# Kernel tuning notes

Hardware: AMD Instinct MI355X
Metric: run time of the kernel (lower is better)

The kernel has to match this reference:

```python
import jax, jax.numpy as jnp
import numpy as np

K = 8
TEMP = 0.05
EPS = 1e-8


def setup_inputs() -> dict:
    key = jax.random.key(0)
    k1, k2, k3, k4, k5, k6 = jax.random.split(key, 6)
    N, D, H = 8192, 1024, 64
    h0 = jax.random.normal(k1, (N, D), dtype=jnp.float32)
    coords = jax.random.uniform(k2, (N, 2), dtype=jnp.float32)
    # tiny MLP params: Linear(2,H) -> ReLU -> Linear(H,1) -> Sigmoid
    W1 = jax.random.normal(k3, (2, H), dtype=jnp.float32) * (1.0 / np.sqrt(2))
    b1 = jnp.zeros((H,), dtype=jnp.float32)
    W2 = jax.random.normal(k4, (H, 1), dtype=jnp.float32) * (1.0 / np.sqrt(H))
    b2 = jnp.zeros((1,), dtype=jnp.float32)
    return {"h0": h0, "coords": coords, "W1": W1, "b1": b1, "W2": W2, "b2": b2}


def reference(h0, coords, W1, b1, W2, b2):
    # pairwise euclidean distances [N, N]
    sq = jnp.sum(coords * coords, axis=-1)                      # [N]
    d2 = sq[:, None] + sq[None, :] - 2.0 * (coords @ coords.T)  # [N, N]
    dist = jnp.sqrt(jnp.maximum(d2, 0.0))

    # k+1 nearest (smallest dist), drop self (index 0)
    _, idx = jax.lax.top_k(-dist, K + 1)                        # [N, K+1]
    knn_idx = idx[:, 1:]                                        # [N, K]

    # gather neighbor features [N, K, D]
    neighbor_feats = h0[knn_idx]

    # cosine similarity between h_i and each neighbor (torch eps semantics)
    num = jnp.einsum('nd,nkd->nk', h0, neighbor_feats)          # [N, K]
    ni = jnp.maximum(jnp.linalg.norm(h0, axis=-1), EPS)         # [N]
    nj = jnp.maximum(jnp.linalg.norm(neighbor_feats, axis=-1), EPS)  # [N, K]
    sim = num / (ni[:, None] * nj)

    # spatial weights from gathered distances
    d_knn = jnp.take_along_axis(dist, knn_idx, axis=1)          # [N, K]
    spatial_w = jnp.exp(-d_knn / TEMP)

    density_input = jnp.stack(
        [sim.mean(axis=1), spatial_w.mean(axis=1)], axis=1)     # [N, 2]

    hmid = jax.nn.relu(density_input @ W1 + b1)
    density = jax.nn.sigmoid(hmid @ W2 + b2)                    # [N, 1]
    return density
```

## Files before the change

### kernel.cpp

```cpp
#include <hip/hip_runtime.h>
#include <math.h>

#define NROWS 8192
#define DIM   1024
#define GRID  64
#define CELLW 0.015625f
#define LPR   16

__device__ __forceinline__ int cell_of(float v) {
    int c = (int)(v * 64.0f);
    return c < 0 ? 0 : (c > 63 ? 63 : c);
}

__device__ __forceinline__ float np_d2(float xi, float yi, float sqi,
                                       float xj, float yj) {
    float sqj = __fadd_rn(__fmul_rn(xj, xj), __fmul_rn(yj, yj));
    float G   = fmaf(yi, yj, __fmul_rn(xi, xj));
    return __fsub_rn(__fadd_rn(sqi, sqj), __fmul_rn(2.0f, G));
}

__global__ __launch_bounds__(1024) void build_grid_kernel(
    const float* __restrict__ coords,
    int* __restrict__ cellStart,
    float4* __restrict__ sxyz) {

    __shared__ int lcnt[4096];
    __shared__ int wsum[16];
    const int t = threadIdx.x;

    for (int i = t; i < 4096; i += 1024) lcnt[i] = 0;
    __syncthreads();

    float2 pc[8]; int pcell[8];
#pragma unroll
    for (int k = 0; k < 8; ++k) {
        int i = t + 1024 * k;
        float2 c = ((const float2*)coords)[i];
        pc[k] = c;
        pcell[k] = cell_of(c.y) * GRID + cell_of(c.x);
        atomicAdd(&lcnt[pcell[k]], 1);
    }
    __syncthreads();

    int c0 = lcnt[t*4+0], c1 = lcnt[t*4+1], c2 = lcnt[t*4+2], c3 = lcnt[t*4+3];
    int s1 = c0, s2 = c0 + c1, s3 = s2 + c2, s4 = s3 + c3;
    int lane = t & 63, wid = t >> 6;
    int inc = s4;
#pragma unroll
    for (int off = 1; off < 64; off <<= 1) {
        int o = __shfl_up(inc, off, 64);
        if (lane >= off) inc += o;
    }
    if (lane == 63) wsum[wid] = inc;
    __syncthreads();
    int wbase = 0;
    for (int w = 0; w < wid; ++w) wbase += wsum[w];
    int excl = wbase + inc - s4;

    cellStart[t*4+0] = excl;
    cellStart[t*4+1] = excl + s1;
    cellStart[t*4+2] = excl + s2;
    cellStart[t*4+3] = excl + s3;
    if (t == 1023) cellStart[4096] = excl + s4;
    lcnt[t*4+0] = excl;
    lcnt[t*4+1] = excl + s1;
    lcnt[t*4+2] = excl + s2;
    lcnt[t*4+3] = excl + s3;
    __syncthreads();

#pragma unroll
    for (int k = 0; k < 8; ++k) {
        int pos = atomicAdd(&lcnt[pcell[k]], 1);
        float x = pc[k].x, y = pc[k].y;
        float sq = __fadd_rn(__fmul_rn(x, x), __fmul_rn(y, y));
        sxyz[pos] = make_float4(x, y, sq, __int_as_float(t + 1024 * k));
    }
}

__global__ __launch_bounds__(256) void knn_kernel(
    const int* __restrict__ cellStart,
    const float4* __restrict__ sxyz,
    unsigned long long* __restrict__ chosen_ws) {

    const int sub = threadIdx.x & (LPR - 1);
    const int g   = (blockIdx.x * 256 + threadIdx.x) / LPR;

    const float4 me = sxyz[g];
    const float xi = me.x, yi = me.y, sqi = me.z;
    const int row = __float_as_int(me.w);
    const int cx = cell_of(xi), cy = cell_of(yi);

    unsigned long long best[10], merged[10];
    int C = 2;
    while (true) {
#pragma unroll
        for (int s = 0; s < 10; ++s) best[s] = ~0ULL;
        int x0 = max(0, cx - C), x1 = min(GRID - 1, cx + C);
        int y0 = max(0, cy - C), y1 = min(GRID - 1, cy + C);
        for (int yy = y0; yy <= y1; ++yy) {
            int s = cellStart[yy * GRID + x0];
            int e = cellStart[yy * GRID + x1 + 1];
            for (int t = s + sub; t < e; t += LPR) {
                float4 c = sxyz[t];
                float d2  = __fsub_rn(__fadd_rn(sqi, c.z),
                                      __fmul_rn(2.0f, fmaf(yi, c.y, __fmul_rn(xi, c.x))));
                float dst = __fsqrt_rn(fmaxf(d2, 0.0f));
                unsigned long long key =
                    ((unsigned long long)__float_as_uint(dst) << 32)
                    | (unsigned int)__float_as_int(c.w);
                if (key < best[9]) {
                    best[9] = key;
#pragma unroll
                    for (int ss = 9; ss >= 1; --ss) {
                        unsigned long long a = best[ss - 1], b = best[ss];
                        unsigned long long lo = a < b ? a : b;
                        unsigned long long hi = a < b ? b : a;
                        best[ss - 1] = lo;
                        best[ss]     = hi;
                    }
                }
            }
        }
#pragma unroll
        for (int r = 0; r < 10; ++r) {
            unsigned long long mn = best[0];
#pragma unroll
            for (int off = 1; off < LPR; off <<= 1) {
                unsigned long long o = __shfl_xor(mn, off, 64);
                mn = (o < mn) ? o : mn;
            }
            if (best[0] == mn) {
#pragma unroll
                for (int ss = 0; ss < 9; ++ss) best[ss] = best[ss + 1];
                best[9] = ~0ULL;
            }
            merged[r] = mn;
        }
        bool done = false;
        if (merged[9] != ~0ULL) {
            float d9 = __uint_as_float((unsigned int)(merged[9] >> 32));
            if (d9 + 1.0e-3f <= (float)C * CELLW) done = true;
        }
        if (done || C >= GRID) break;
        C <<= 1; if (C > GRID) C = GRID;
    }

    if (sub == 0) {
        unsigned long long* o = chosen_ws + (size_t)row * 10;
#pragma unroll
        for (int r = 0; r < 10; ++r) o[r] = merged[r];
    }
}

__global__ __launch_bounds__(256) void gather_final_kernel(
    const float* __restrict__ h0,
    const float* __restrict__ coords,
    const unsigned long long* __restrict__ chosen_ws,
    const float4* __restrict__ sxyz,
    const float* __restrict__ W1, const float* __restrict__ b1,
    const float* __restrict__ W2, const float* __restrict__ b2,
    float* __restrict__ out) {

    const int wid  = threadIdx.x >> 6;
    const int lane = threadIdx.x & 63;
    const int bid  = blockIdx.x;
    const int grp  = (bid & 7) * (gridDim.x / 8) + (bid >> 3);
    const int g    = grp * 4 + wid;
    const int row  = __float_as_int(sxyz[g].w);

    const unsigned long long* ch = chosen_ws + (size_t)row * 10;
    unsigned long long chosen[10];
    int jidx[10];
#pragma unroll
    for (int r = 0; r < 10; ++r) {
        chosen[r] = ch[r];
        jidx[r]   = (int)(chosen[r] & 0xFFFFFFFFu);
    }

    const float4* hi = (const float4*)(h0 + (size_t)row * DIM);

    float p[11];
    float q[10];
#pragma unroll
    for (int s = 0; s < 11; ++s) p[s] = 0.f;
#pragma unroll
    for (int s = 0; s < 10; ++s) q[s] = 0.f;

    for (int t = 0; t < 4; ++t) {
        float4 av = hi[lane + 64 * t];
        p[10] += av.x * av.x + av.y * av.y + av.z * av.z + av.w * av.w;
#pragma unroll
        for (int s = 0; s < 10; ++s) {
            float4 b = ((const float4*)(h0 + (size_t)jidx[s] * DIM))[lane + 64 * t];
            p[s] += av.x * b.x + av.y * b.y + av.z * b.z + av.w * b.w;
            q[s] += b.x * b.x + b.y * b.y + b.z * b.z + b.w * b.w;
        }
    }

#pragma unroll
    for (int s = 0; s < 11; ++s) {
        float v = p[s];
#pragma unroll
        for (int off = 1; off < 64; off <<= 1) v += __shfl_xor(v, off, 64);
        p[s] = v;
    }
#pragma unroll
    for (int s = 0; s < 10; ++s) {
        float v = q[s];
#pragma unroll
        for (int off = 1; off < 64; off <<= 1) v += __shfl_xor(v, off, 64);
        q[s] = v;
    }

    const float2 ci = ((const float2*)coords)[row];
    const float xi = ci.x, yi = ci.y;
    const float sqi = __fadd_rn(__fmul_rn(xi, xi), __fmul_rn(yi, yi));

    auto clamped_d2 = [&](unsigned long long key) -> float {
        int j = (int)(key & 0xFFFFFFFFu);
        float2 cj = ((const float2*)coords)[j];
        return fmaxf(np_d2(xi, yi, sqi, cj.x, cj.y), 0.0f);
    };
    const float m0 = clamped_d2(chosen[0]);
    const float m1 = clamped_d2(chosen[1]);
    const float m2 = clamped_d2(chosen[2]);
    const float m8 = clamped_d2(chosen[8]);
    const float m9 = clamped_d2(chosen[9]);

    const float WIN = 2.0e-6f;
    const bool fpair = (m1 - m0) <= WIN;
    const bool ftri  = fpair && ((m2 - m0) <= WIN);
    const bool f89   = (m9 - m8) <= WIN;

    float wd[3];
    wd[0] = ftri ? (1.f / 3.f) : (fpair ? 0.5f : 1.0f);
    wd[1] = ftri ? (1.f / 3.f) : (fpair ? 0.5f : 0.0f);
    wd[2] = ftri ? (1.f / 3.f) : 0.0f;
    const float wc0 = f89 ? 0.5f : 1.0f;
    const float wc1 = f89 ? 0.5f : 0.0f;

    const float ni = fmaxf(sqrtf(p[10]), 1e-8f);

    float sim[10], sw[10];
#pragma unroll
    for (int r = 0; r < 10; ++r) {
        float dst = __uint_as_float((unsigned int)(chosen[r] >> 32));
        float nj  = fmaxf(sqrtf(q[r]), 1e-8f);
        sim[r] = p[r] / (ni * nj);
        sw[r]  = expf(__fdiv_rn(-dst, 0.05f));
    }

    float Ssim = 0.f, Ssw = 0.f;
#pragma unroll
    for (int r = 0; r < 9; ++r) { Ssim += sim[r]; Ssw += sw[r]; }

    const float w1a = W1[lane], w1b = W1[64 + lane];
    const float b1l = b1[lane], w2l = W2[lane], b2s = b2[0];

    float outacc = 0.f;
#pragma unroll
    for (int d = 0; d < 3; ++d) {
#pragma unroll
        for (int c = 0; c < 2; ++c) {
            float wgt = wd[d] * (c ? wc1 : wc0);
            float simsum = Ssim - sim[d] + (c ? (sim[9] - sim[8]) : 0.f);
            float swsum  = Ssw  - sw[d]  + (c ? (sw[9]  - sw[8])  : 0.f);
            float di0 = simsum * 0.125f;
            float di1 = swsum  * 0.125f;
            float hm = fmaxf(di0 * w1a + di1 * w1b + b1l, 0.f);
            float v  = hm * w2l;
#pragma unroll
            for (int off = 1; off < 64; off <<= 1) v += __shfl_xor(v, off, 64);
            float z = v + b2s;
            outacc += wgt * (1.f / (1.f + expf(-z)));
        }
    }

    if (lane == 0) out[row] = outacc;
}

extern "C" void kernel_launch(void* const* d_in, const int* in_sizes, int n_in,
                              void* d_out, int out_size, void* d_ws, size_t ws_size,
                              hipStream_t stream) {
    const float* h0     = (const float*)d_in[0];
    const float* coords = (const float*)d_in[1];
    const float* W1     = (const float*)d_in[2];
    const float* b1     = (const float*)d_in[3];
    const float* W2     = (const float*)d_in[4];
    const float* b2     = (const float*)d_in[5];
    float* out = (float*)d_out;

    char* ws = (char*)d_ws;
    unsigned long long* chosen_ws = (unsigned long long*)(ws);
    float4* sxyz      = (float4*)(ws + 1015808);
    int*    cellStart = (int*)(ws + 1146880);

    build_grid_kernel  <<<1, 1024, 0, stream>>>(coords, cellStart, sxyz);
    knn_kernel         <<<NROWS * LPR / 256, 256, 0, stream>>>(cellStart, sxyz, chosen_ws);
    gather_final_kernel<<<NROWS / 4, 256, 0, stream>>>(h0, coords, chosen_ws, sxyz,
                                                       W1, b1, W2, b2, out);
}
```

Baseline: 58.37 us.

## Precompute row norms inside knn kernel and drop neighbor norm reductions in gather

```diff
diff --git a/kernel.cpp b/kernel.cpp
--- a/kernel.cpp
+++ b/kernel.cpp
@@ -78,9 +78,31 @@
 }
 
 __global__ __launch_bounds__(256) void knn_kernel(
+    const float* __restrict__ h0,
     const int* __restrict__ cellStart,
     const float4* __restrict__ sxyz,
-    unsigned long long* __restrict__ chosen_ws) {
+    unsigned long long* __restrict__ chosen_ws,
+    float* __restrict__ norms) {
+
+    {
+        const int wv   = threadIdx.x >> 6;
+        const int lane = threadIdx.x & 63;
+        int rbase = blockIdx.x * 16 + wv * 4;
+#pragma unroll
+        for (int k = 0; k < 4; ++k) {
+            int row = rbase + k;
+            const float4* hp = (const float4*)(h0 + (size_t)row * DIM);
+            float acc = 0.f;
+#pragma unroll
+            for (int t = 0; t < 4; ++t) {
+                float4 v = hp[lane + 64 * t];
+                acc += v.x * v.x + v.y * v.y + v.z * v.z + v.w * v.w;
+            }
+#pragma unroll
+            for (int off = 1; off < 64; off <<= 1) acc += __shfl_xor(acc, off, 64);
+            if (lane == 0) norms[row] = sqrtf(acc);
+        }
+    }
 
     const int sub = threadIdx.x & (LPR - 1);
     const int g   = (blockIdx.x * 256 + threadIdx.x) / LPR;
@@ -157,6 +179,7 @@
     const float* __restrict__ coords,
     const unsigned long long* __restrict__ chosen_ws,
     const float4* __restrict__ sxyz,
+    const float* __restrict__ norms,
     const float* __restrict__ W1, const float* __restrict__ b1,
     const float* __restrict__ W2, const float* __restrict__ b2,
     float* __restrict__ out) {
@@ -170,46 +193,35 @@
 
     const unsigned long long* ch = chosen_ws + (size_t)row * 10;
     unsigned long long chosen[10];
-    int jidx[10];
+    const float4* hj[10];
 #pragma unroll
     for (int r = 0; r < 10; ++r) {
         chosen[r] = ch[r];
-        jidx[r]   = (int)(chosen[r] & 0xFFFFFFFFu);
+        hj[r] = (const float4*)(h0 + (size_t)(int)(chosen[r] & 0xFFFFFFFFu) * DIM);
     }
 
     const float4* hi = (const float4*)(h0 + (size_t)row * DIM);
 
-    float p[11];
-    float q[10];
-#pragma unroll
-    for (int s = 0; s < 11; ++s) p[s] = 0.f;
-#pragma unroll
-    for (int s = 0; s < 10; ++s) q[s] = 0.f;
-
+    float p[10];
+#pragma unroll
+    for (int s = 0; s < 10; ++s) p[s] = 0.f;
+
+#pragma unroll
     for (int t = 0; t < 4; ++t) {
         float4 av = hi[lane + 64 * t];
-        p[10] += av.x * av.x + av.y * av.y + av.z * av.z + av.w * av.w;
 #pragma unroll
         for (int s = 0; s < 10; ++s) {
-            float4 b = ((const float4*)(h0 + (size_t)jidx[s] * DIM))[lane + 64 * t];
+            float4 b = hj[s][lane + 64 * t];
             p[s] += av.x * b.x + av.y * b.y + av.z * b.z + av.w * b.w;
-            q[s] += b.x * b.x + b.y * b.y + b.z * b.z + b.w * b.w;
-        }
-    }
-
-#pragma unroll
-    for (int s = 0; s < 11; ++s) {
+        }
+    }
+
+#pragma unroll
+    for (int s = 0; s < 10; ++s) {
         float v = p[s];
 #pragma unroll
         for (int off = 1; off < 64; off <<= 1) v += __shfl_xor(v, off, 64);
         p[s] = v;
-    }
-#pragma unroll
-    for (int s = 0; s < 10; ++s) {
-        float v = q[s];
-#pragma unroll
-        for (int off = 1; off < 64; off <<= 1) v += __shfl_xor(v, off, 64);
-        q[s] = v;
     }
 
     const float2 ci = ((const float2*)coords)[row];
@@ -239,13 +251,14 @@
     const float wc0 = f89 ? 0.5f : 1.0f;
     const float wc1 = f89 ? 0.5f : 0.0f;
 
-    const float ni = fmaxf(sqrtf(p[10]), 1e-8f);
+    const float ni = fmaxf(norms[row], 1e-8f);
 
     float sim[10], sw[10];
 #pragma unroll
     for (int r = 0; r < 10; ++r) {
+        int   j   = (int)(chosen[r] & 0xFFFFFFFFu);
         float dst = __uint_as_float((unsigned int)(chosen[r] >> 32));
-        float nj  = fmaxf(sqrtf(q[r]), 1e-8f);
+        float nj  = fmaxf(norms[j], 1e-8f);
         sim[r] = p[r] / (ni * nj);
         sw[r]  = expf(__fdiv_rn(-dst, 0.05f));
     }
@@ -292,11 +305,13 @@
 
     char* ws = (char*)d_ws;
     unsigned long long* chosen_ws = (unsigned long long*)(ws);
+    float*  norms     = (float*)(ws + 655360);
     float4* sxyz      = (float4*)(ws + 1015808);
     int*    cellStart = (int*)(ws + 1146880);
 
     build_grid_kernel  <<<1, 1024, 0, stream>>>(coords, cellStart, sxyz);
-    knn_kernel         <<<NROWS * LPR / 256, 256, 0, stream>>>(cellStart, sxyz, chosen_ws);
+    knn_kernel         <<<NROWS * LPR / 256, 256, 0, stream>>>(h0, cellStart, sxyz,
+                                                               chosen_ws, norms);
     gather_final_kernel<<<NROWS / 4, 256, 0, stream>>>(h0, coords, chosen_ws, sxyz,
-                                                       W1, b1, W2, b2, out);
-}
+                                                       norms, W1, b1, W2, b2, out);
+}
```

New measurement: 62.68 us. 1.07x slower.
